# Optimization experiments

Hardware: AMD Instinct MI355X
Metric: run time of the kernel (lower is better)

## Reference

```python
import jax, jax.numpy as jnp
import numpy as np

B, G, H = 16, 1708, 5


def setup_inputs() -> dict:
    key = jax.random.key(0)
    k0, k1, k2, k3 = jax.random.split(key, 4)
    x = jax.random.normal(k0, (B, G), dtype=jnp.float32)
    # xavier_normal on (H, G, 1): std = gain*sqrt(2/(fan_in+fan_out)) ~ gain*sqrt(2/G)
    std_qk = 5.0 * np.sqrt(2.0 / (G + 1))   # gain=5 for WQ, WK
    std_v = 1.0 * np.sqrt(2.0 / (G + 1))    # gain=1 for WV
    WQ = jax.random.normal(k1, (H, G, 1), dtype=jnp.float32) * std_qk
    WK = jax.random.normal(k2, (H, G, 1), dtype=jnp.float32) * std_qk
    WV = jax.random.normal(k3, (H, G, 1), dtype=jnp.float32) * std_v
    W0 = jnp.ones((H,), dtype=jnp.float32)  # torch.Tensor(n_head*[1])
    return {"x": x, "WQ": WQ, "WK": WK, "WV": WV, "W0": W0}


def reference(x, WQ, WK, WV, W0):
    # x: (B, G); WQ/WK/WV: (H, G, 1); W0: (H,)
    g = x.shape[1]
    off_diag = 1.0 - jnp.eye(g, dtype=x.dtype)  # mask applied AFTER softmax
    head_outs = []
    for h in range(WQ.shape[0]):  # small fixed head loop keeps peak memory low
        q = x * WQ[h, :, 0]  # (B, G)
        k = x * WK[h, :, 0]  # (B, G)
        v = x * WV[h, :, 0]  # (B, G)
        # scores[b,i,j] = q[b,i] * k[b,j]  (broadcast outer product, not dot-product)
        scores = q[:, :, None] * k[:, None, :]  # (B, G, G)
        z = jax.nn.softmax(scores, axis=2) * off_diag
        head_outs.append(jnp.einsum('bij,bj->bi', z, v))  # (B, G)
    out_seq = jnp.stack(head_outs, axis=-1)  # (B, G, H)
    return jnp.einsum('bgh,h->bg', out_seq, W0)  # (B, G)
```

## Files before the change

### kernel.cpp

```cpp
#include <hip/hip_runtime.h>

constexpr int B  = 16;
constexpr int G  = 1708;
constexpr int H  = 5;
constexpr int M1 = 17;
constexpr int TPB = 512;
constexpr int NW  = TPB / 64;
constexpr int RR  = NW * 8;
constexpr int TILES = (G + TPB - 1) / TPB;

#define LOG2E 1.4426950408889634f


__device__ __forceinline__ float fast_exp(float x) {
#if __has_builtin(__builtin_amdgcn_exp2f)
    return __builtin_amdgcn_exp2f(x * LOG2E);
#else
    return __expf(x);
#endif
}

__constant__ float INVFACT[M1] = {
    (float)(1.0),                    (float)(1.0),
    (float)(1.0 / 2.0),              (float)(1.0 / 6.0),
    (float)(1.0 / 24.0),             (float)(1.0 / 120.0),
    (float)(1.0 / 720.0),            (float)(1.0 / 5040.0),
    (float)(1.0 / 40320.0),          (float)(1.0 / 362880.0),
    (float)(1.0 / 3628800.0),        (float)(1.0 / 39916800.0),
    (float)(1.0 / 479001600.0),      (float)(1.0 / 6227020800.0),
    (float)(1.0 / 87178291200.0),    (float)(1.0 / 1307674368000.0),
    (float)(1.0 / 20922789888000.0)
};

__global__ __launch_bounds__(TPB)
void fused_kernel(const float* __restrict__ x,
                  const float* __restrict__ WQ,
                  const float* __restrict__ WK,
                  const float* __restrict__ WV,
                  const float* __restrict__ W0,
                  float* __restrict__ out)
{
    __shared__ float xs[G];
    __shared__ float red[H][RR][2 * M1];
    __shared__ float mom[H][2 * M1];

    const int tile = blockIdx.x;
    const int b    = blockIdx.y;
    const int tid  = threadIdx.x;
    const int lane = tid & 63;
    const int wave = tid >> 6;

    const float* __restrict__ xb = x + b * G;
    for (int t = tid; t < G; t += TPB) xs[t] = xb[t];
    __syncthreads();

#pragma unroll 1
    for (int h = 0; h < H; ++h) {
        const float* __restrict__ wk = WK + h * G;
        const float* __restrict__ wv = WV + h * G;

        float S[M1], T[M1];
#pragma unroll
        for (int m = 0; m < M1; ++m) { S[m] = 0.f; T[m] = 0.f; }

        for (int t = tid; t < G; t += TPB) {
            const float xj = xs[t];
            const float k  = xj * wk[t];
            const float v  = xj * wv[t];
            const float k2 = k * k;
            const float k4 = k2 * k2;
            float p0 = 1.f, p1 = k, p2 = k2, p3 = k2 * k;
#pragma unroll
            for (int gblk = 0; gblk < 4; ++gblk) {
                const int base = gblk * 4;
                S[base + 0] += p0; T[base + 0] = fmaf(v, p0, T[base + 0]); p0 *= k4;
                S[base + 1] += p1; T[base + 1] = fmaf(v, p1, T[base + 1]); p1 *= k4;
                S[base + 2] += p2; T[base + 2] = fmaf(v, p2, T[base + 2]); p2 *= k4;
                S[base + 3] += p3; T[base + 3] = fmaf(v, p3, T[base + 3]); p3 *= k4;
            }
            S[16] += p0; T[16] = fmaf(v, p0, T[16]);
        }

#pragma unroll
        for (int m = 0; m < M1; ++m) {
#pragma unroll
            for (int off = 8; off <= 32; off <<= 1) {
                S[m] += __shfl_xor(S[m], off, 64);
                T[m] += __shfl_xor(T[m], off, 64);
            }
        }
        if (lane < 8) {
            const int r = wave * 8 + lane;
#pragma unroll
            for (int m = 0; m < M1; ++m) {
                red[h][r][m]      = S[m];
                red[h][r][M1 + m] = T[m];
            }
        }
    }
    __syncthreads();

    if (tid < H * 2 * M1) {
        const int h = tid / (2 * M1);
        const int c = tid % (2 * M1);
        float s0 = 0.f, s1 = 0.f, s2 = 0.f, s3 = 0.f;
#pragma unroll
        for (int r = 0; r < RR; r += 4) {
            s0 += red[h][r + 0][c];
            s1 += red[h][r + 1][c];
            s2 += red[h][r + 2][c];
            s3 += red[h][r + 3][c];
        }
        const int m = (c < M1) ? c : (c - M1);
        mom[h][c] = ((s0 + s1) + (s2 + s3)) * INVFACT[m];
    }
    __syncthreads();

    const int i = tile * TPB + tid;
    if (i < G) {
        const float xi = xs[i];
        float acc = 0.f;
#pragma unroll
        for (int h = 0; h < H; ++h) {
            const float q = xi * WQ[h * G + i];

            float D = mom[h][M1 - 1];
            float N = mom[h][2 * M1 - 1];
#pragma unroll
            for (int m = M1 - 2; m >= 0; --m) {
                D = fmaf(D, q, mom[h][m]);
                N = fmaf(N, q, mom[h][M1 + m]);
            }

            const float k   = xi * WK[h * G + i];
            const float v   = xi * WV[h * G + i];
            const float eii = fast_exp(q * k);
            acc = fmaf(W0[h], (N - eii * v) / D, acc);
        }
        out[b * G + i] = acc;
    }
}

extern "C" void kernel_launch(void* const* d_in, const int* in_sizes, int n_in,
                              void* d_out, int out_size, void* d_ws, size_t ws_size,
                              hipStream_t stream) {
    const float* x  = (const float*)d_in[0];
    const float* WQ = (const float*)d_in[1];
    const float* WK = (const float*)d_in[2];
    const float* WV = (const float*)d_in[3];
    const float* W0 = (const float*)d_in[4];
    float* out = (float*)d_out;

    dim3 grid(TILES, B);
    fused_kernel<<<grid, TPB, 0, stream>>>(x, WQ, WK, WV, W0, out);
}
```

Measured before the change: 78.10 us.

## Assign one wave per head for moment sums and shrink row tiles to 128

The moment accumulation now gives each head its own wavefront (5 waves, 320 threads), so all heads are summed concurrently instead of in a sequential head loop across 8 waves. The x shared-memory staging is removed and x is read straight from global memory. Output rows per block drop from 512 to 128, which gives 14 tiles per batch and more blocks, but every block still recomputes the full moment sums over G. The intent is to cut per-block latency and raise occupancy, at the cost of more redundant reduction work across blocks.

```diff
diff --git a/kernel.cpp b/kernel.cpp
--- a/kernel.cpp
+++ b/kernel.cpp
@@ -1,13 +1,12 @@
 #include <hip/hip_runtime.h>
 
-constexpr int B  = 16;
-constexpr int G  = 1708;
-constexpr int H  = 5;
-constexpr int M1 = 17;
-constexpr int TPB = 512;
-constexpr int NW  = TPB / 64;
-constexpr int RR  = NW * 8;
-constexpr int TILES = (G + TPB - 1) / TPB;
+constexpr int B    = 16;
+constexpr int G    = 1708;
+constexpr int H    = 5;
+constexpr int M1   = 17;
+constexpr int TPB  = 320;
+constexpr int ROWS = 128;
+constexpr int TILES = (G + ROWS - 1) / ROWS;
 
 #define LOG2E 1.4426950408889634f
 
@@ -40,62 +39,53 @@
                   const float* __restrict__ W0,
                   float* __restrict__ out)
 {
-    __shared__ float xs[G];
-    __shared__ float red[H][RR][2 * M1];
-    __shared__ float mom[H][2 * M1];
+    __shared__ float red[H][8][2 * M1];
+    __shared__ float mom[H * 2 * M1];
 
-    const int tile = blockIdx.x;
     const int b    = blockIdx.y;
     const int tid  = threadIdx.x;
     const int lane = tid & 63;
     const int wave = tid >> 6;
 
-    const float* __restrict__ xb = x + b * G;
-    for (int t = tid; t < G; t += TPB) xs[t] = xb[t];
-    __syncthreads();
+    const float* __restrict__ xb = x  + b * G;
+    const float* __restrict__ wk = WK + wave * G;
+    const float* __restrict__ wv = WV + wave * G;
 
-#pragma unroll 1
-    for (int h = 0; h < H; ++h) {
-        const float* __restrict__ wk = WK + h * G;
-        const float* __restrict__ wv = WV + h * G;
+    float S[M1], T[M1];
+#pragma unroll
+    for (int m = 0; m < M1; ++m) { S[m] = 0.f; T[m] = 0.f; }
 
-        float S[M1], T[M1];
+    for (int t = lane; t < G; t += 64) {
+        const float xj = xb[t];
+        const float k  = xj * wk[t];
+        const float v  = xj * wv[t];
+        const float k2 = k * k;
+        const float k4 = k2 * k2;
+        float p0 = 1.f, p1 = k, p2 = k2, p3 = k2 * k;
 #pragma unroll
-        for (int m = 0; m < M1; ++m) { S[m] = 0.f; T[m] = 0.f; }
-
-        for (int t = tid; t < G; t += TPB) {
-            const float xj = xs[t];
-            const float k  = xj * wk[t];
-            const float v  = xj * wv[t];
-            const float k2 = k * k;
-            const float k4 = k2 * k2;
-            float p0 = 1.f, p1 = k, p2 = k2, p3 = k2 * k;
-#pragma unroll
-            for (int gblk = 0; gblk < 4; ++gblk) {
-                const int base = gblk * 4;
-                S[base + 0] += p0; T[base + 0] = fmaf(v, p0, T[base + 0]); p0 *= k4;
-                S[base + 1] += p1; T[base + 1] = fmaf(v, p1, T[base + 1]); p1 *= k4;
-                S[base + 2] += p2; T[base + 2] = fmaf(v, p2, T[base + 2]); p2 *= k4;
-                S[base + 3] += p3; T[base + 3] = fmaf(v, p3, T[base + 3]); p3 *= k4;
-            }
-            S[16] += p0; T[16] = fmaf(v, p0, T[16]);
+        for (int gblk = 0; gblk < 4; ++gblk) {
+            const int base = gblk * 4;
+            S[base + 0] += p0; T[base + 0] = fmaf(v, p0, T[base + 0]); p0 *= k4;
+            S[base + 1] += p1; T[base + 1] = fmaf(v, p1, T[base + 1]); p1 *= k4;
+            S[base + 2] += p2; T[base + 2] = fmaf(v, p2, T[base + 2]); p2 *= k4;
+            S[base + 3] += p3; T[base + 3] = fmaf(v, p3, T[base + 3]); p3 *= k4;
         }
+        S[16] += p0; T[16] = fmaf(v, p0, T[16]);
+    }
 
 #pragma unroll
+    for (int m = 0; m < M1; ++m) {
+#pragma unroll
+        for (int off = 8; off <= 32; off <<= 1) {
+            S[m] += __shfl_xor(S[m], off, 64);
+            T[m] += __shfl_xor(T[m], off, 64);
+        }
+    }
+    if (lane < 8) {
+#pragma unroll
         for (int m = 0; m < M1; ++m) {
-#pragma unroll
-            for (int off = 8; off <= 32; off <<= 1) {
-                S[m] += __shfl_xor(S[m], off, 64);
-                T[m] += __shfl_xor(T[m], off, 64);
-            }
-        }
-        if (lane < 8) {
-            const int r = wave * 8 + lane;
-#pragma unroll
-            for (int m = 0; m < M1; ++m) {
-                red[h][r][m]      = S[m];
-                red[h][r][M1 + m] = T[m];
-            }
+            red[wave][lane][m]      = S[m];
+            red[wave][lane][M1 + m] = T[m];
         }
     }
     __syncthreads();
@@ -103,33 +93,32 @@
     if (tid < H * 2 * M1) {
         const int h = tid / (2 * M1);
         const int c = tid % (2 * M1);
-        float s0 = 0.f, s1 = 0.f, s2 = 0.f, s3 = 0.f;
+        float s0 = 0.f, s1 = 0.f;
 #pragma unroll
-        for (int r = 0; r < RR; r += 4) {
+        for (int r = 0; r < 8; r += 2) {
             s0 += red[h][r + 0][c];
             s1 += red[h][r + 1][c];
-            s2 += red[h][r + 2][c];
-            s3 += red[h][r + 3][c];
         }
         const int m = (c < M1) ? c : (c - M1);
-        mom[h][c] = ((s0 + s1) + (s2 + s3)) * INVFACT[m];
+        mom[tid] = (s0 + s1) * INVFACT[m];
     }
     __syncthreads();
 
-    const int i = tile * TPB + tid;
-    if (i < G) {
-        const float xi = xs[i];
+    const int i = blockIdx.x * ROWS + tid;
+    if (tid < ROWS && i < G) {
+        const float xi = xb[i];
         float acc = 0.f;
 #pragma unroll
         for (int h = 0; h < H; ++h) {
+            const float* __restrict__ mp = mom + h * (2 * M1);
             const float q = xi * WQ[h * G + i];
 
-            float D = mom[h][M1 - 1];
-            float N = mom[h][2 * M1 - 1];
+            float D = mp[M1 - 1];
+            float N = mp[2 * M1 - 1];
 #pragma unroll
             for (int m = M1 - 2; m >= 0; --m) {
-                D = fmaf(D, q, mom[h][m]);
-                N = fmaf(N, q, mom[h][M1 + m]);
+                D = fmaf(D, q, mp[m]);
+                N = fmaf(N, q, mp[M1 + m]);
             }
 
             const float k   = xi * WK[h * G + i];
```

Result: faster. 75.88 us (-2.8%).
